# Performance work log

Measured on AMD Instinct MI355X. Metric: run time of the kernel, lower is better.

The kernel has to match this reference:

```python
import jax, jax.numpy as jnp
import numpy as np

B, S, HID, NH = 2, 2048, 2048, 16
DH = HID // NH  # 128


def _rope_tables(seq_len, dim, dtype=jnp.float32):
    inv_freq = 1.0 / (10000.0 ** (jnp.arange(0, dim, 2, dtype=jnp.float32) / dim))
    t = jnp.arange(seq_len, dtype=jnp.float32)
    freqs = jnp.einsum('i,j->ij', t, inv_freq)          # [S, dim/2]
    emb = jnp.concatenate([freqs, freqs], axis=-1)       # [S, dim]
    return jnp.cos(emb)[None, None].astype(dtype), jnp.sin(emb)[None, None].astype(dtype)


def _rotate_half(x):
    x1, x2 = x[..., : x.shape[-1] // 2], x[..., x.shape[-1] // 2 :]
    return jnp.concatenate([-x2, x1], axis=-1)


def setup_inputs() -> dict:
    key = jax.random.key(0)
    ks = jax.random.split(key, 6)
    hidden_states = jax.random.normal(ks[0], (B, S, HID), dtype=jnp.float32)
    scale = 1.0 / np.sqrt(HID)
    Wq = jax.random.normal(ks[1], (HID, HID), dtype=jnp.float32) * scale
    Wk = jax.random.normal(ks[2], (HID, HID), dtype=jnp.float32) * scale
    Wv = jax.random.normal(ks[3], (HID, HID), dtype=jnp.float32) * scale
    Wo = jax.random.normal(ks[4], (HID, HID), dtype=jnp.float32) * scale
    bq = jnp.zeros((HID,), jnp.float32)
    bk = jnp.zeros((HID,), jnp.float32)
    bv = jnp.zeros((HID,), jnp.float32)
    bo = jnp.zeros((HID,), jnp.float32)
    # causal additive mask [1,1,S,S]
    causal = jnp.tril(jnp.ones((S, S), dtype=bool))
    attention_mask = jnp.where(causal, 0.0, -1e9).astype(jnp.float32)[None, None]
    return dict(hidden_states=hidden_states, attention_mask=attention_mask,
                Wq=Wq, bq=bq, Wk=Wk, bk=bk, Wv=Wv, bv=bv, Wo=Wo, bo=bo)


def reference(hidden_states, attention_mask, Wq, bq, Wk, bk, Wv, bv, Wo, bo):
    b, s, _ = hidden_states.shape
    # torch Linear: x @ W.T + b
    q = (hidden_states @ Wq.T + bq).reshape(b, s, NH, DH).transpose(0, 2, 1, 3)
    k = (hidden_states @ Wk.T + bk).reshape(b, s, NH, DH).transpose(0, 2, 1, 3)
    v = (hidden_states @ Wv.T + bv).reshape(b, s, NH, DH).transpose(0, 2, 1, 3)
    cos, sin = _rope_tables(s, DH)
    q = q * cos + _rotate_half(q) * sin
    k = k * cos + _rotate_half(k) * sin
    scores = jnp.einsum('bhqd,bhkd->bhqk', q * (DH ** -0.5), k)
    scores = scores + attention_mask
    probs = jax.nn.softmax(scores, axis=-1)  # dropout: eval mode (identity)
    out = jnp.einsum('bhqk,bhkd->bhqd', probs, v)
    out = out.transpose(0, 2, 1, 3).reshape(b, s, HID)
    return out @ Wo.T + bo
```

## Files before the change

kernel.cpp:

```cpp
#include <hip/hip_runtime.h>
#include <hip/hip_bf16.h>
#include <cstdint>
#include <cstddef>

#define BB 2
#define SS 2048
#define HH 2048
#define NHH 16
#define DHH 128

using f32x4  = __attribute__((ext_vector_type(4))) float;
using bf16x8 = __attribute__((ext_vector_type(8))) __bf16;
using bf16x4 = __attribute__((ext_vector_type(4))) __bf16;
using bfloat = __bf16;

__device__ inline void gload_lds16(const void* g, void* l) {
    __builtin_amdgcn_global_load_lds(
        (const __attribute__((address_space(1))) void*)g,
        (__attribute__((address_space(3))) void*)l, 16, 0, 0);
}

__device__ inline f32x4 mfma16(bf16x8 a, bf16x8 b, f32x4 c) {
    return __builtin_amdgcn_mfma_f32_16x16x32_bf16(a, b, c, 0, 0, 0);
}

template <int CTRL>
__device__ inline float dpp_max_step(float x) {
    int y = __builtin_amdgcn_update_dpp(0, __builtin_bit_cast(int, x), CTRL, 0xf, 0xf, false);
    return fmaxf(x, __builtin_bit_cast(float, y));
}
__device__ inline float rowmax16(float x) {
    x = dpp_max_step<0x121>(x);
    x = dpp_max_step<0x122>(x);
    x = dpp_max_step<0x124>(x);
    x = dpp_max_step<0x128>(x);
    return x;
}

__global__ void prep_all(const float* __restrict__ hs,
                         const float* __restrict__ w0, const float* __restrict__ w1,
                         const float* __restrict__ w2, const float* __restrict__ w3,
                         bfloat* __restrict__ xb,
                         bfloat* __restrict__ d0, bfloat* __restrict__ d1,
                         bfloat* __restrict__ d2, bfloat* __restrict__ d3,
                         float* __restrict__ cosT, float* __restrict__ sinT) {
    const int bid = blockIdx.x, tid = threadIdx.x;
    if (bid < 8192 + 16384) {
        const float* s;
        bfloat* d;
        int i;
        if (bid < 8192) {
            s = hs; d = xb; i = bid * 256 + tid;
        } else {
            int b2 = bid - 8192, sel = b2 >> 12;
            s = sel == 0 ? w0 : sel == 1 ? w1 : sel == 2 ? w2 : w3;
            d = sel == 0 ? d0 : sel == 1 ? d1 : sel == 2 ? d2 : d3;
            i = (b2 & 4095) * 256 + tid;
        }
        float4 v = reinterpret_cast<const float4*>(s)[i];
        bf16x4 o;
        o[0] = (bfloat)v.x; o[1] = (bfloat)v.y; o[2] = (bfloat)v.z; o[3] = (bfloat)v.w;
        reinterpret_cast<bf16x4*>(d)[i] = o;
    } else {
        int i = (bid - 24576) * 256 + tid;
        int s = i >> 6, j = i & 63;
        float invf = powf(10000.0f, -(float)j / 64.0f);
        float ang = (float)s * invf;
        cosT[i] = cosf(ang);
        sinT[i] = sinf(ang);
    }
}

__device__ __forceinline__ void kloop128(const bfloat* __restrict__ Ag,
                                         const bfloat* __restrict__ Bg,
                                         f32x4 (&acc)[4][4]) {
    constexpr int K = HH, NT = K / 32;
    __shared__ bfloat As[2][128 * 32];
    __shared__ bfloat Bs[2][128 * 32];
    const int t = threadIdx.x, l = t & 63, lr = l & 15, lg = l >> 4;
    const int w = t >> 6, wm = (w >> 1) * 64, wc = w & 1;
    const int ubase = t & ~63;

    auto stage = [&](int buf, int kt) {
#pragma unroll
        for (int i = 0; i < 2; i++) {
            int idx = i * 256 + t;
            int r = idx >> 2, u = idx & 3;
            int us = u ^ (r & 3) ^ ((r >> 2) & 1);
            gload_lds16(Ag + (size_t)r * K + kt * 32 + us * 8,
                        &As[buf][(i * 256 + ubase) * 8]);
        }
#pragma unroll
        for (int i = 0; i < 2; i++) {
            int idx = i * 256 + t;
            int r = idx >> 2, u = idx & 3;
            int us = u ^ (r & 3) ^ ((r >> 2) & 1);
            gload_lds16(Bg + (size_t)r * K + kt * 32 + us * 8,
                        &Bs[buf][(i * 256 + ubase) * 8]);
        }
    };

    stage(0, 0);

#pragma unroll 1
    for (int kt = 0; kt < NT; ++kt) {
        const int buf = kt & 1;
        if (kt + 1 < NT) {
            stage(buf ^ 1, kt + 1);
            asm volatile("s_waitcnt vmcnt(4)" ::: "memory");
        } else {
            asm volatile("s_waitcnt vmcnt(0)" ::: "memory");
        }
        __builtin_amdgcn_s_barrier();
        __builtin_amdgcn_sched_barrier(0);

        const bfloat* A_ = As[buf];
        const bfloat* B_ = Bs[buf];
        bf16x8 af[4], bfr[4];
#pragma unroll
        for (int mi = 0; mi < 4; mi++) {
            int row = wm + mi * 16 + lr;
            int us = lg ^ (row & 3) ^ ((row >> 2) & 1);
            af[mi] = *reinterpret_cast<const bf16x8*>(&A_[row * 32 + us * 8]);
        }
#pragma unroll
        for (int ni = 0; ni < 4; ni++) {
            int row = wc * 32 + (ni & 1) * 16 + (ni >> 1) * 64 + lr;
            int us = lg ^ (row & 3) ^ ((row >> 2) & 1);
            bfr[ni] = *reinterpret_cast<const bf16x8*>(&B_[row * 32 + us * 8]);
        }
        __builtin_amdgcn_s_setprio(1);
#pragma unroll
        for (int mi = 0; mi < 4; mi++)
#pragma unroll
            for (int ni = 0; ni < 4; ni++)
                acc[mi][ni] = mfma16(af[mi], bfr[ni], acc[mi][ni]);
        __builtin_amdgcn_s_setprio(0);
        __builtin_amdgcn_sched_barrier(0);
        __builtin_amdgcn_s_barrier();
    }
}

__global__ __launch_bounds__(256, 4)
void gemm_qkv(const bfloat* __restrict__ A,
              const bfloat* __restrict__ Bq, const bfloat* __restrict__ Bk,
              const bfloat* __restrict__ Bv,
              const float* __restrict__ bq, const float* __restrict__ bk,
              const float* __restrict__ bv,
              bfloat* __restrict__ Qo, bfloat* __restrict__ Ko, bfloat* __restrict__ Vto,
              const float* __restrict__ cosT, const float* __restrict__ sinT) {
    constexpr int K = HH, N = HH;
    const int bid = blockIdx.x;
    const int xcd = bid & 7, idx = bid >> 3;
    const int by = xcd * 6 + (idx >> 5);
    const int bx = idx & 31;
    const int sel = by >> 4;
    const bfloat* Bt = sel == 0 ? Bq : sel == 1 ? Bk : Bv;
    const float* bias = sel == 0 ? bq : sel == 1 ? bk : bv;
    const int m0 = bx * 128, n0 = (by & 15) * 128;

    f32x4 acc[4][4] = {};
    kloop128(A + (size_t)m0 * K, Bt + (size_t)n0 * K, acc);

    const int t = threadIdx.x, l = t & 63, lr = l & 15, lg = l >> 4;
    const int w = t >> 6, wm = (w >> 1) * 64, wc = w & 1;

    if (sel == 2) {
#pragma unroll
        for (int mi = 0; mi < 4; mi++) {
            int row = m0 + wm + mi * 16 + lg * 4;
#pragma unroll
            for (int ni = 0; ni < 4; ni++) {
                int cb = wc * 32 + (ni & 1) * 16 + (ni >> 1) * 64;
                int col = n0 + cb + lr;
                float bv_ = bias[col];
#pragma unroll
                for (int j = 0; j < 4; j++) {
                    int r = row + j;
                    Vto[((size_t)((r >> 11) * HH + col)) * SS + (r & (SS - 1))] =
                        (bfloat)(acc[mi][ni][j] + bv_);
                }
            }
        }
    } else {
        bfloat* C = sel == 0 ? Qo : Ko;
        const float qs = sel == 0 ? 0.088388347648318447f : 1.0f;
#pragma unroll
        for (int mi = 0; mi < 4; mi++) {
            int row = m0 + wm + mi * 16 + lg * 4;
#pragma unroll
            for (int ni = 0; ni < 2; ni++) {
                int d = wc * 32 + ni * 16 + lr;
                int col1 = n0 + d, col2 = col1 + 64;
                float b1 = bias[col1], b2 = bias[col2];
#pragma unroll
                for (int j = 0; j < 4; j++) {
                    int r = row + j, s = r & (SS - 1);
                    float c  = cosT[s * 64 + d];
                    float sn = sinT[s * 64 + d];
                    float x1 = acc[mi][ni][j] + b1;
                    float x2 = acc[mi][ni + 2][j] + b2;
                    C[(size_t)r * N + col1] = (bfloat)((x1 * c - x2 * sn) * qs);
                    C[(size_t)r * N + col2] = (bfloat)((x2 * c + x1 * sn) * qs);
                }
            }
        }
    }
}

__global__ __launch_bounds__(256, 4)
void gemm_out(const bfloat* __restrict__ A, const bfloat* __restrict__ Bt,
              const float* __restrict__ bias, float* __restrict__ C) {
    constexpr int K = HH, N = HH;
    const int bid = blockIdx.x;
    const int xcd = bid & 7, idx = bid >> 3;
    const int by = xcd * 2 + (idx >> 5);
    const int bx = idx & 31;
    const int m0 = bx * 128, n0 = by * 128;

    f32x4 acc[4][4] = {};
    kloop128(A + (size_t)m0 * K, Bt + (size_t)n0 * K, acc);

    const int t = threadIdx.x, l = t & 63, lr = l & 15, lg = l >> 4;
    const int w = t >> 6, wm = (w >> 1) * 64, wc = w & 1;
#pragma unroll
    for (int mi = 0; mi < 4; mi++) {
        int row = m0 + wm + mi * 16 + lg * 4;
#pragma unroll
        for (int ni = 0; ni < 4; ni++) {
            int cb = wc * 32 + (ni & 1) * 16 + (ni >> 1) * 64;
            int col = n0 + cb + lr;
            float bv = bias[col];
#pragma unroll
            for (int j = 0; j < 4; j++)
                C[(size_t)(row + j) * N + col] = acc[mi][ni][j] + bv;
        }
    }
}

__global__ __launch_bounds__(256, 4)
void attn_fwd(const bfloat* __restrict__ Q, const bfloat* __restrict__ K,
              const bfloat* __restrict__ Vt, bfloat* __restrict__ O) {
    __shared__ bfloat Ks[64 * 128];
    __shared__ bfloat Vs[128 * 64];
    __shared__ bfloat Pw[4][16 * 64];

    const int t = threadIdx.x, w = t >> 6, l = t & 63;
    const int lr = l & 15, lg = l >> 4;
    const int swz = (lr & 7) << 4;

    const int f = blockIdx.x;
    const int xcd = f & 7, slot = f >> 3;
    const int bh = xcd + 8 * (slot >> 5);
    const int qidx = 31 - (slot & 31);
    const int b = bh >> 4, h = bh & 15;
    const int q0 = qidx * 64 + w * 16;

    const size_t bo_ = (size_t)b * SS * HH + (size_t)h * DHH;
    const bfloat* Qp = Q + bo_;
    const bfloat* Kp = K + bo_;
    const bfloat* Vp = Vt + (size_t)(b * NHH + h) * DHH * SS;
    bfloat* Op = O + bo_;

    auto stage = [&](int kv0) {
#pragma unroll
        for (int i = 0; i < 4; i++) {
            int Ub = (i * 4 + w) * 64;
            int U = Ub + l;
            int r = U >> 4;
            int u = (U & 15) ^ (r & 7);
            gload_lds16(Kp + (size_t)(kv0 + r) * HH + u * 8, &Ks[Ub * 8]);
        }
#pragma unroll
        for (int i = 0; i < 4; i++) {
            int Ub = (i * 4 + w) * 64;
            int U = Ub + l;
            int r = U >> 3;
            int u = (U & 7) ^ (r & 7);
            gload_lds16(Vp + (size_t)r * SS + kv0 + u * 8, &Vs[Ub * 8]);
        }
    };

    bf16x8 qf[4];
#pragma unroll
    for (int kt = 0; kt < 4; kt++)
        qf[kt] = *reinterpret_cast<const bf16x8*>(Qp + (size_t)(q0 + lr) * HH + kt * 32 + lg * 8);

    bf16x8 ones;
#pragma unroll
    for (int e = 0; e < 8; e++) ones[e] = (bfloat)1.0f;

    f32x4 o[8] = {};
    f32x4 lsv = {};
    float m[4];
#pragma unroll
    for (int j = 0; j < 4; j++) m[j] = -1e30f;

    const int nkv = qidx + 1;

    for (int kv = 0; kv < nkv; ++kv) {
        stage(kv * 64);
        __syncthreads();

        const char* KB = (const char*)&Ks[0];
        const char* VB = (const char*)&Vs[0];

        f32x4 sc[4] = {};
        __builtin_amdgcn_s_setprio(1);
#pragma unroll
        for (int kt = 0; kt < 4; kt++) {
            const int col = (kt * 64 + lg * 16);
#pragma unroll
            for (int kb = 0; kb < 4; kb++) {
                bf16x8 kf = *reinterpret_cast<const bf16x8*>(
                    KB + (kb * 16 + lr) * 256 + (col ^ swz));
                sc[kb] = mfma16(qf[kt], kf, sc[kb]);
            }
        }
        __builtin_amdgcn_s_setprio(0);

        const bool diag = (kv == nkv - 1);
        float p[4][4], alpha[4];
        bool ga = false;
#pragma unroll
        for (int j = 0; j < 4; j++) {
            float v0 = sc[0][j], v1 = sc[1][j], v2 = sc[2][j], v3 = sc[3][j];
            if (diag) {
                int qr = q0 + lg * 4 + j;
                int k0 = kv * 64 + lr;
                if (k0      > qr) v0 = -1e30f;
                if (k0 + 16 > qr) v1 = -1e30f;
                if (k0 + 32 > qr) v2 = -1e30f;
                if (k0 + 48 > qr) v3 = -1e30f;
            }
            float mx = rowmax16(fmaxf(fmaxf(v0, v1), fmaxf(v2, v3)));
            bool grow = mx > m[j] + 8.0f;
            float mn = grow ? mx : m[j];
            alpha[j] = grow ? __expf(m[j] - mn) : 1.0f;
            m[j] = mn;
            ga = ga || grow;
            p[0][j] = __expf(v0 - mn);
            p[1][j] = __expf(v1 - mn);
            p[2][j] = __expf(v2 - mn);
            p[3][j] = __expf(v3 - mn);
        }
        if (__any(ga)) {
#pragma unroll
            for (int j = 0; j < 4; j++) {
                lsv[j] *= alpha[j];
#pragma unroll
                for (int nt = 0; nt < 8; nt++) o[nt][j] *= alpha[j];
            }
        }

        char* pwb = (char*)&Pw[w][0];
#pragma unroll
        for (int j = 0; j < 4; j++) {
            int q = lg * 4 + j;
            int qs = (q & 7) << 4;
#pragma unroll
            for (int kb = 0; kb < 4; kb++)
                *(bfloat*)(pwb + q * 128 + ((kb * 32 + lr * 2) ^ qs)) = (bfloat)p[kb][j];
        }
        asm volatile("s_waitcnt lgkmcnt(0)" ::: "memory");
        __builtin_amdgcn_sched_barrier(0);

        const char* pwr = (const char*)&Pw[w][0];
        bf16x8 pa0 = *reinterpret_cast<const bf16x8*>(pwr + lr * 128 + ((lg * 16) ^ swz));
        bf16x8 pa1 = *reinterpret_cast<const bf16x8*>(pwr + lr * 128 + ((64 + lg * 16) ^ swz));
        __builtin_amdgcn_s_setprio(1);
        lsv = mfma16(pa0, ones, lsv);
        lsv = mfma16(pa1, ones, lsv);
#pragma unroll
        for (int nt = 0; nt < 8; nt++) {
            const char* vb = VB + (nt * 16 + lr) * 128;
            bf16x8 vf0 = *reinterpret_cast<const bf16x8*>(vb + ((lg * 16) ^ swz));
            bf16x8 vf1 = *reinterpret_cast<const bf16x8*>(vb + ((64 + lg * 16) ^ swz));
            o[nt] = mfma16(pa0, vf0, o[nt]);
            o[nt] = mfma16(pa1, vf1, o[nt]);
        }
        __builtin_amdgcn_s_setprio(0);
        __syncthreads();
    }

#pragma unroll
    for (int j = 0; j < 4; j++) {
        float inv = 1.0f / lsv[j];
        int row = q0 + lg * 4 + j;
#pragma unroll
        for (int nt = 0; nt < 8; nt++)
            Op[(size_t)row * HH + nt * 16 + lr] = (bfloat)(o[nt][j] * inv);
    }
}

extern "C" void kernel_launch(void* const* d_in, const int* in_sizes, int n_in,
                              void* d_out, int out_size, void* d_ws, size_t ws_size,
                              hipStream_t stream) {
    (void)in_sizes; (void)n_in; (void)out_size; (void)ws_size;
    const float* hs = (const float*)d_in[0];
    const float* Wq = (const float*)d_in[2];
    const float* bq = (const float*)d_in[3];
    const float* Wk = (const float*)d_in[4];
    const float* bk = (const float*)d_in[5];
    const float* Wv = (const float*)d_in[6];
    const float* bv = (const float*)d_in[7];
    const float* Wo = (const float*)d_in[8];
    const float* bo = (const float*)d_in[9];

    char* ws = (char*)d_ws;
    size_t off = 0;
    auto alloc = [&](size_t bytes) { void* p = ws + off; off += (bytes + 255) & ~(size_t)255; return p; };
    const size_t MK = (size_t)BB * SS * HH;
    const size_t NK = (size_t)HH * HH;

    bfloat* Xb  = (bfloat*)alloc(MK * 2);
    bfloat* Wqb = (bfloat*)alloc(NK * 2);
    bfloat* Wkb = (bfloat*)alloc(NK * 2);
    bfloat* Wvb = (bfloat*)alloc(NK * 2);
    bfloat* Wob = (bfloat*)alloc(NK * 2);
    bfloat* Qb  = (bfloat*)alloc(MK * 2);
    bfloat* Kb  = (bfloat*)alloc(MK * 2);
    bfloat* Vtb = (bfloat*)alloc(MK * 2);
    float*  cosT = (float*)alloc((size_t)SS * 64 * 4);
    float*  sinT = (float*)alloc((size_t)SS * 64 * 4);
    bfloat* AOb = Xb;

    prep_all<<<8192 + 16384 + 512, 256, 0, stream>>>(
        hs, Wq, Wk, Wv, Wo, Xb, Wqb, Wkb, Wvb, Wob, cosT, sinT);

    gemm_qkv<<<1536, 256, 0, stream>>>(
        Xb, Wqb, Wkb, Wvb, bq, bk, bv, Qb, Kb, Vtb, cosT, sinT);

    attn_fwd<<<1024, 256, 0, stream>>>(Qb, Kb, Vtb, AOb);

    gemm_out<<<512, 256, 0, stream>>>(AOb, Wob, bo, (float*)d_out);
}
```

Before: 313.1 us.

## Drop XCD-aware block swizzle and vectorize transposed V stores

Replaces the XCD-aware block index remapping in the QKV and output GEMMs with a plain 2D grid, so blocks on the same XCD no longer share B-tiles in L2 by construction. Separately, the V-transpose epilogue now packs four consecutive sequence positions into one 8-byte bf16x4 store instead of four scalar 2-byte stores. The vector store cuts the number of scattered write transactions. Removing the swizzle may reduce L2 locality on the 8-XCD part.

```diff
diff --git a/kernel.cpp b/kernel.cpp
--- a/kernel.cpp
+++ b/kernel.cpp
@@ -150,14 +150,10 @@
               bfloat* __restrict__ Qo, bfloat* __restrict__ Ko, bfloat* __restrict__ Vto,
               const float* __restrict__ cosT, const float* __restrict__ sinT) {
     constexpr int K = HH, N = HH;
-    const int bid = blockIdx.x;
-    const int xcd = bid & 7, idx = bid >> 3;
-    const int by = xcd * 6 + (idx >> 5);
-    const int bx = idx & 31;
-    const int sel = by >> 4;
+    const int sel = blockIdx.y >> 4;
     const bfloat* Bt = sel == 0 ? Bq : sel == 1 ? Bk : Bv;
     const float* bias = sel == 0 ? bq : sel == 1 ? bk : bv;
-    const int m0 = bx * 128, n0 = (by & 15) * 128;
+    const int m0 = blockIdx.x * 128, n0 = (blockIdx.y & 15) * 128;
 
     f32x4 acc[4][4] = {};
     kloop128(A + (size_t)m0 * K, Bt + (size_t)n0 * K, acc);
@@ -169,17 +165,19 @@
 #pragma unroll
         for (int mi = 0; mi < 4; mi++) {
             int row = m0 + wm + mi * 16 + lg * 4;
+            int bb = row >> 11;
+            int s0 = row & (SS - 1);
 #pragma unroll
             for (int ni = 0; ni < 4; ni++) {
                 int cb = wc * 32 + (ni & 1) * 16 + (ni >> 1) * 64;
                 int col = n0 + cb + lr;
                 float bv_ = bias[col];
-#pragma unroll
-                for (int j = 0; j < 4; j++) {
-                    int r = row + j;
-                    Vto[((size_t)((r >> 11) * HH + col)) * SS + (r & (SS - 1))] =
-                        (bfloat)(acc[mi][ni][j] + bv_);
-                }
+                bf16x4 pack;
+#pragma unroll
+                for (int j = 0; j < 4; j++)
+                    pack[j] = (bfloat)(acc[mi][ni][j] + bv_);
+                *reinterpret_cast<bf16x4*>(
+                    &Vto[((size_t)(bb * HH + col)) * SS + s0]) = pack;
             }
         }
     } else {
@@ -212,11 +210,7 @@
 void gemm_out(const bfloat* __restrict__ A, const bfloat* __restrict__ Bt,
               const float* __restrict__ bias, float* __restrict__ C) {
     constexpr int K = HH, N = HH;
-    const int bid = blockIdx.x;
-    const int xcd = bid & 7, idx = bid >> 3;
-    const int by = xcd * 2 + (idx >> 5);
-    const int bx = idx & 31;
-    const int m0 = bx * 128, n0 = by * 128;
+    const int m0 = blockIdx.x * 128, n0 = blockIdx.y * 128;
 
     f32x4 acc[4][4] = {};
     kloop128(A + (size_t)m0 * K, Bt + (size_t)n0 * K, acc);
@@ -428,10 +422,10 @@
     prep_all<<<8192 + 16384 + 512, 256, 0, stream>>>(
         hs, Wq, Wk, Wv, Wo, Xb, Wqb, Wkb, Wvb, Wob, cosT, sinT);
 
-    gemm_qkv<<<1536, 256, 0, stream>>>(
+    gemm_qkv<<<dim3(32, 48), 256, 0, stream>>>(
         Xb, Wqb, Wkb, Wvb, bq, bk, bv, Qb, Kb, Vtb, cosT, sinT);
 
     attn_fwd<<<1024, 256, 0, stream>>>(Qb, Kb, Vtb, AOb);
 
-    gemm_out<<<512, 256, 0, stream>>>(AOb, Wob, bo, (float*)d_out);
-}
+    gemm_out<<<dim3(32, 16), 256, 0, stream>>>(AOb, Wob, bo, (float*)d_out);
+}
```

After: 308.1 us. No clear change (-1.6%).
